# Kernel tuning notes

Hardware: AMD Instinct MI355X
Metric: run time of the kernel (lower is better)

## Reference

```python
import jax, jax.numpy as jnp
import numpy as np
from jax import lax

K = 16        # patch_size / kernel_size
S = 16        # stride
EMB = 768     # embed_dim
CIN = 3


def setup_inputs() -> dict:
    key = jax.random.key(0)
    k1, k2, k3, k4, k5 = jax.random.split(key, 5)
    B, H, W = 64, 384, 384
    pixel_values = jax.random.normal(k1, (B, CIN, H, W), jnp.float32)
    # offset conv: Conv2d(3, 2*K*K, kernel=K, stride=K); small init so offsets stay moderate
    offset_w = jax.random.normal(k2, (2 * K * K, CIN, K, K), jnp.float32) * 0.01
    offset_b = jax.random.normal(k3, (2 * K * K,), jnp.float32) * 0.01
    # deformable projection: DeformConv2d(3, 768, kernel=K, stride=K)
    proj_w = jax.random.normal(k4, (EMB, CIN, K, K), jnp.float32) * 0.02
    proj_b = jax.random.normal(k5, (EMB,), jnp.float32) * 0.02
    return {"pixel_values": pixel_values, "offset_w": offset_w, "offset_b": offset_b,
            "proj_w": proj_w, "proj_b": proj_b}


def _bilinear_gather(img, py, px):
    """img: [B,C,H,W]; py,px: [B,K,K,HO,WO] float sample coords.
    Returns [B,C,K,K,HO,WO] with zero padding outside the image (torchvision semantics)."""
    B, C, H, W = img.shape
    shp = py.shape
    y0 = jnp.floor(py); x0 = jnp.floor(px)
    wy1 = py - y0; wy0 = 1.0 - wy1
    wx1 = px - x0; wx0 = 1.0 - wx1
    imgf = img.reshape(B, C, H * W)

    def corner(yy, xx, w):
        valid = (yy >= 0) & (yy < H) & (xx >= 0) & (xx < W)
        yi = jnp.clip(yy, 0, H - 1).astype(jnp.int32)
        xi = jnp.clip(xx, 0, W - 1).astype(jnp.int32)
        idx = (yi * W + xi).reshape(B, -1)                       # [B, N]
        v = jnp.take_along_axis(imgf, idx[:, None, :], axis=2)   # [B, C, N]
        return v * (jnp.where(valid, w, 0.0)).reshape(B, 1, -1)

    val = (corner(y0, x0, wy0 * wx0) + corner(y0, x0 + 1, wy0 * wx1)
           + corner(y0 + 1, x0, wy1 * wx0) + corner(y0 + 1, x0 + 1, wy1 * wx1))
    return val.reshape((B, C) + shp[1:])


def reference(pixel_values, offset_w, offset_b, proj_w, proj_b):
    B, C, H, W = pixel_values.shape
    HO, WO = H // S, W // S
    # offset conv (dense, stride=patch, VALID padding)
    offset = lax.conv_general_dilated(pixel_values, offset_w, (S, S), 'VALID',
                                      dimension_numbers=('NCHW', 'OIHW', 'NCHW'))
    offset = offset + offset_b[None, :, None, None]              # [B, 2*K*K, HO, WO]
    off = offset.reshape(B, K * K, 2, HO, WO)
    dy = off[:, :, 0].reshape(B, K, K, HO, WO)
    dx = off[:, :, 1].reshape(B, K, K, HO, WO)
    # base sampling grid: p = (ho*S + i + dy, wo*S + j + dx)
    base_y = (jnp.arange(HO, dtype=jnp.float32) * S)[None, None, None, :, None] \
             + jnp.arange(K, dtype=jnp.float32)[None, :, None, None, None]
    base_x = (jnp.arange(WO, dtype=jnp.float32) * S)[None, None, None, None, :] \
             + jnp.arange(K, dtype=jnp.float32)[None, None, :, None, None]
    py = base_y + dy
    px = base_x + dx
    sampled = _bilinear_gather(pixel_values, py, px)             # [B, C, K, K, HO, WO]
    out = jnp.einsum('bcijhw,ocij->bohw', sampled, proj_w) + proj_b[None, :, None, None]
    # flatten(2).transpose(1,2) -> [B, HO*WO, EMB]
    return out.reshape(B, EMB, HO * WO).transpose(0, 2, 1)
```

## Files before the change

### kernel.cpp

```cpp
#include <hip/hip_runtime.h>
#include <stdint.h>

typedef __bf16 bf16x8 __attribute__((ext_vector_type(8)));
typedef float  f32x4  __attribute__((ext_vector_type(4)));

#define HH 384
#define WW 384
#define NPIX (HH*WW)
#define NC 3
#define NPATCH 576
#define EMB 768
#define PLEN 768
#define MLOC 32
#define KSTEPS 24
#define NLOC (64*576)
#define NT1 4
#define NT2 6
#define W1_UNITS (32*KSTEPS*64)
#define W2_UNITS (48*KSTEPS*64)
#define W2_OFF   (W1_UNITS*8)

__device__ __forceinline__ uint16_t f2bf(float f) {
    uint32_t u = __builtin_bit_cast(uint32_t, f);
    u += 0x7FFFu + ((u >> 16) & 1u);
    return (uint16_t)(u >> 16);
}
__device__ __forceinline__ uint32_t pk2(float a, float b) {
    return (uint32_t)f2bf(a) | ((uint32_t)f2bf(b) << 16);
}

__global__ __launch_bounds__(256)
void convert_weights(const float* __restrict__ offw, const float* __restrict__ projw,
                     uint16_t* __restrict__ wz) {
    int u = blockIdx.x * 256 + threadIdx.x;
    const float* src;
    int uu;
    if (u < W1_UNITS) { src = offw; uu = u; }
    else              { src = projw; uu = u - W1_UNITS; }
    int lane = uu & 63;
    int t    = uu >> 6;
    int ks   = t % KSTEPS;
    int nt   = t / KSTEPS;
    int n    = nt * 16 + (lane & 15);
    int k0   = ks * 32 + (lane >> 4) * 8;
    const float4* s4 = (const float4*)(src + (size_t)n * PLEN + k0);
    float4 v0 = s4[0], v1 = s4[1];
    uint4 w;
    w.x = pk2(v0.x, v0.y); w.y = pk2(v0.z, v0.w);
    w.z = pk2(v1.x, v1.y); w.w = pk2(v1.z, v1.w);
    *(uint4*)(wz + (size_t)u * 8) = w;
}

template<bool USE_WS>
__global__ __launch_bounds__(512, 4)
void fused_kernel(const float* __restrict__ pix,
                  const float* __restrict__ offw,
                  const float* __restrict__ offb,
                  const float* __restrict__ projw,
                  const float* __restrict__ projb,
                  const uint16_t* __restrict__ wz,
                  float* __restrict__ out) {
    __shared__ __align__(16) uint16_t As[MLOC][PLEN];

    const int tid  = threadIdx.x;
    const int wv   = tid >> 6;
    const int lane = tid & 63;
    const int lr   = lane & 15;
    const int lg   = lane >> 4;

    int bid = (int)blockIdx.x;
    bid = (bid & 7) * 144 + (bid >> 3);

    const int loc0 = bid * MLOC;
    const int bimg = loc0 / NPATCH;
    const int p0   = loc0 - bimg * NPATCH;
    const float* __restrict__ pb = pix + (size_t)bimg * NC * NPIX;

    #pragma unroll
    for (int uu = 0; uu < 6; ++uu) {
        int unit = tid + uu * 512;
        int loc  = unit / 96;
        int k8   = (unit - loc * 96) * 8;
        int c  = k8 >> 8;
        int i  = (k8 >> 4) & 15;
        int j  = k8 & 15;
        int p  = p0 + loc;
        int ho = p / 24;
        int wo = p - ho * 24;
        const float* g = pb + ((size_t)c * HH + ho * 16 + i) * WW + wo * 16 + j;
        float4 v0 = *(const float4*)g;
        float4 v1 = *(const float4*)(g + 4);
        uint4 w;
        w.x = pk2(v0.x, v0.y); w.y = pk2(v0.z, v0.w);
        w.z = pk2(v1.x, v1.y); w.w = pk2(v1.z, v1.w);
        *(uint4*)&As[loc][k8 ^ ((loc & 7) << 3)] = w;
    }

    const int sw0 = (lr & 7) << 3;

    auto ldb1 = [&](int ntg, int ks) -> bf16x8 {
        if (USE_WS) {
            return *(const bf16x8*)(wz + ((size_t)((ntg * KSTEPS + ks) * 64 + lane)) * 8);
        } else {
            int n = ntg * 16 + lr;
            const float4* s4 = (const float4*)(offw + (size_t)n * PLEN + ks * 32 + lg * 8);
            float4 v0 = s4[0], v1 = s4[1];
            uint4 uq = {pk2(v0.x,v0.y), pk2(v0.z,v0.w), pk2(v1.x,v1.y), pk2(v1.z,v1.w)};
            return __builtin_bit_cast(bf16x8, uq);
        }
    };
    bf16x8 b1a[NT1], b1b[NT1];
    #pragma unroll
    for (int nt = 0; nt < NT1; ++nt) b1a[nt] = ldb1(wv * NT1 + nt, 0);
    __syncthreads();

    f32x4 acc1[2][NT1];
    #pragma unroll
    for (int nt = 0; nt < NT1; ++nt) {
        float bz = offb[(wv * NT1 + nt) * 16 + lr];
        f32x4 z = {bz, bz, bz, bz};
        acc1[0][nt] = z; acc1[1][nt] = z;
    }
    #pragma unroll 1
    for (int ks2 = 0; ks2 < KSTEPS / 2; ++ks2) {
        const int ks0 = ks2 * 2;
        {
            #pragma unroll
            for (int nt = 0; nt < NT1; ++nt) b1b[nt] = ldb1(wv * NT1 + nt, ks0 + 1);
            int ke = (ks0 * 32 + lg * 8) ^ sw0;
            bf16x8 a0 = *(const bf16x8*)&As[lr][ke];
            bf16x8 a1 = *(const bf16x8*)&As[16 + lr][ke];
            __builtin_amdgcn_s_setprio(1);
            #pragma unroll
            for (int nt = 0; nt < NT1; ++nt) {
                acc1[0][nt] = __builtin_amdgcn_mfma_f32_16x16x32_bf16(a0, b1a[nt], acc1[0][nt], 0, 0, 0);
                acc1[1][nt] = __builtin_amdgcn_mfma_f32_16x16x32_bf16(a1, b1a[nt], acc1[1][nt], 0, 0, 0);
            }
            __builtin_amdgcn_s_setprio(0);
        }
        {
            int ksn = (ks0 + 2 < KSTEPS) ? ks0 + 2 : 0;
            #pragma unroll
            for (int nt = 0; nt < NT1; ++nt) b1a[nt] = ldb1(wv * NT1 + nt, ksn);
            int ke = ((ks0 + 1) * 32 + lg * 8) ^ sw0;
            bf16x8 a0 = *(const bf16x8*)&As[lr][ke];
            bf16x8 a1 = *(const bf16x8*)&As[16 + lr][ke];
            __builtin_amdgcn_s_setprio(1);
            #pragma unroll
            for (int nt = 0; nt < NT1; ++nt) {
                acc1[0][nt] = __builtin_amdgcn_mfma_f32_16x16x32_bf16(a0, b1b[nt], acc1[0][nt], 0, 0, 0);
                acc1[1][nt] = __builtin_amdgcn_mfma_f32_16x16x32_bf16(a1, b1b[nt], acc1[1][nt], 0, 0, 0);
            }
            __builtin_amdgcn_s_setprio(0);
        }
    }
    __syncthreads();

    const int even = ((lane & 1) == 0);
    float dyg[2][2][4], dxg[2][2][4];
    #pragma unroll
    for (int nt = 0; nt < NT1; ++nt)
      #pragma unroll
      for (int mt = 0; mt < 2; ++mt)
        #pragma unroll
        for (int r = 0; r < 4; ++r) {
            float v  = acc1[mt][nt][r];
            float pv = __shfl_xor(v, 1);
            if ((nt < 2) == (even != 0)) {
                int s = nt & 1;
                dyg[s][mt][r] = even ? v  : pv;
                dxg[s][mt][r] = even ? pv : v;
            }
        }

    const int ntb  = wv * NT1 + (even ? 0 : 2);
    const int qlow = lr >> 1;
    #pragma unroll
    for (int s = 0; s < 2; ++s) {
        int q  = (ntb + s) * 8 + qlow;
        int qi = q >> 4;
        int qj = q & 15;
        #pragma unroll
        for (int mt = 0; mt < 2; ++mt)
          #pragma unroll
          for (int r = 0; r < 4; ++r) {
            int locl = mt * 16 + lg * 4 + r;
            int p  = p0 + locl;
            int ho = p / 24;
            int wo = p - ho * 24;
            float py = (float)(ho * 16 + qi) + dyg[s][mt][r];
            float px = (float)(wo * 16 + qj) + dxg[s][mt][r];
            float y0f = floorf(py), x0f = floorf(px);
            float wy1 = py - y0f, wy0 = 1.f - wy1;
            float wx1 = px - x0f, wx0 = 1.f - wx1;
            int y0 = (int)y0f, x0 = (int)x0f;
            float s0 = 0.f, s1 = 0.f, s2 = 0.f;
            #pragma unroll
            for (int cy = 0; cy < 2; ++cy) {
                int yy = y0 + cy;
                if ((unsigned)yy < (unsigned)HH) {
                    float wy = cy ? wy1 : wy0;
                    #pragma unroll
                    for (int cx = 0; cx < 2; ++cx) {
                        int xx = x0 + cx;
                        if ((unsigned)xx < (unsigned)WW) {
                            float w = wy * (cx ? wx1 : wx0);
                            const float* cp = pb + yy * WW + xx;
                            s0 += w * cp[0];
                            s1 += w * cp[NPIX];
                            s2 += w * cp[2 * NPIX];
                        }
                    }
                }
            }
            int swl = (locl & 7) << 3;
            As[locl][(      q) ^ swl] = f2bf(s0);
            As[locl][(256 + q) ^ swl] = f2bf(s1);
            As[locl][(512 + q) ^ swl] = f2bf(s2);
          }
    }

    auto ldb2 = [&](int ntg, int ks) -> bf16x8 {
        if (USE_WS) {
            return *(const bf16x8*)(wz + W2_OFF + ((size_t)((ntg * KSTEPS + ks) * 64 + lane)) * 8);
        } else {
            int n = ntg * 16 + lr;
            const float4* s4 = (const float4*)(projw + (size_t)n * PLEN + ks * 32 + lg * 8);
            float4 v0 = s4[0], v1 = s4[1];
            uint4 uq = {pk2(v0.x,v0.y), pk2(v0.z,v0.w), pk2(v1.x,v1.y), pk2(v1.z,v1.w)};
            return __builtin_bit_cast(bf16x8, uq);
        }
    };
    bf16x8 b2a[NT2], b2b[NT2];
    #pragma unroll
    for (int nt = 0; nt < NT2; ++nt) b2a[nt] = ldb2(wv * NT2 + nt, 0);
    __syncthreads();

    f32x4 acc2[2][NT2];
    #pragma unroll
    for (int nt = 0; nt < NT2; ++nt) {
        float bz = projb[(wv * NT2 + nt) * 16 + lr];
        f32x4 z = {bz, bz, bz, bz};
        acc2[0][nt] = z; acc2[1][nt] = z;
    }
    #pragma unroll 1
    for (int ks2 = 0; ks2 < KSTEPS / 2; ++ks2) {
        const int ks0 = ks2 * 2;
        {
            #pragma unroll
            for (int nt = 0; nt < NT2; ++nt) b2b[nt] = ldb2(wv * NT2 + nt, ks0 + 1);
            int ke = (ks0 * 32 + lg * 8) ^ sw0;
            bf16x8 a0 = *(const bf16x8*)&As[lr][ke];
            bf16x8 a1 = *(const bf16x8*)&As[16 + lr][ke];
            __builtin_amdgcn_s_setprio(1);
            #pragma unroll
            for (int nt = 0; nt < NT2; ++nt) {
                acc2[0][nt] = __builtin_amdgcn_mfma_f32_16x16x32_bf16(a0, b2a[nt], acc2[0][nt], 0, 0, 0);
                acc2[1][nt] = __builtin_amdgcn_mfma_f32_16x16x32_bf16(a1, b2a[nt], acc2[1][nt], 0, 0, 0);
            }
            __builtin_amdgcn_s_setprio(0);
        }
        {
            int ksn = (ks0 + 2 < KSTEPS) ? ks0 + 2 : 0;
            #pragma unroll
            for (int nt = 0; nt < NT2; ++nt) b2a[nt] = ldb2(wv * NT2 + nt, ksn);
            int ke = ((ks0 + 1) * 32 + lg * 8) ^ sw0;
            bf16x8 a0 = *(const bf16x8*)&As[lr][ke];
            bf16x8 a1 = *(const bf16x8*)&As[16 + lr][ke];
            __builtin_amdgcn_s_setprio(1);
            #pragma unroll
            for (int nt = 0; nt < NT2; ++nt) {
                acc2[0][nt] = __builtin_amdgcn_mfma_f32_16x16x32_bf16(a0, b2b[nt], acc2[0][nt], 0, 0, 0);
                acc2[1][nt] = __builtin_amdgcn_mfma_f32_16x16x32_bf16(a1, b2b[nt], acc2[1][nt], 0, 0, 0);
            }
            __builtin_amdgcn_s_setprio(0);
        }
    }

    #pragma unroll
    for (int mt = 0; mt < 2; ++mt)
      #pragma unroll
      for (int r = 0; r < 4; ++r) {
        int flat = loc0 + mt * 16 + lg * 4 + r;
        float* op = out + (size_t)flat * EMB;
        #pragma unroll
        for (int nt = 0; nt < NT2; ++nt)
            op[(wv * NT2 + nt) * 16 + lr] = acc2[mt][nt][r];
      }
}

extern "C" void kernel_launch(void* const* d_in, const int* in_sizes, int n_in,
                              void* d_out, int out_size, void* d_ws, size_t ws_size,
                              hipStream_t stream) {
    const float* pix   = (const float*)d_in[0];
    const float* offw  = (const float*)d_in[1];
    const float* offb  = (const float*)d_in[2];
    const float* projw = (const float*)d_in[3];
    const float* projb = (const float*)d_in[4];
    float* out = (float*)d_out;
    uint16_t* wz = (uint16_t*)d_ws;

    const size_t ws_needed = (size_t)(W1_UNITS + W2_UNITS) * 16;
    dim3 grid(NLOC / MLOC);

    if (ws_size >= ws_needed) {
        convert_weights<<<(W1_UNITS + W2_UNITS) / 256, 256, 0, stream>>>(offw, projw, wz);
        fused_kernel<true><<<grid, 512, 0, stream>>>(pix, offw, offb, projw, projb, wz, out);
    } else {
        fused_kernel<false><<<grid, 512, 0, stream>>>(pix, offw, offb, projw, projb, wz, out);
    }
}
```

Baseline: 206.3 us.

## Make fused kernel persistent with atomic tile counter and sample from LDS

Launches a fixed 512-block persistent grid that pulls 32-location tiles from a global atomic counter, reset by a memset each call, instead of one block per tile. Bilinear samples whose corners fall inside the tile's own patches are now read from the bf16 patch copy already staged in LDS rather than from global fp32 pixels. Sampled values are held in registers until after a barrier and then written back to LDS, which removes the earlier barrier placement. This trades tail-effect and launch overhead for an atomic per tile, an extra memset, and lower-precision (bf16) inputs to the sampling.

```diff
diff --git a/kernel.cpp b/kernel.cpp
--- a/kernel.cpp
+++ b/kernel.cpp
@@ -14,11 +14,14 @@
 #define MLOC 32
 #define KSTEPS 24
 #define NLOC (64*576)
+#define NTILES (NLOC/MLOC)
 #define NT1 4
 #define NT2 6
 #define W1_UNITS (32*KSTEPS*64)
 #define W2_UNITS (48*KSTEPS*64)
 #define W2_OFF   (W1_UNITS*8)
+#define CTR_OFF  ((size_t)(W1_UNITS + W2_UNITS) * 16)
+#define PERSIST_BLOCKS 512
 
 __device__ __forceinline__ uint16_t f2bf(float f) {
     uint32_t u = __builtin_bit_cast(uint32_t, f);
@@ -27,6 +30,9 @@
 }
 __device__ __forceinline__ uint32_t pk2(float a, float b) {
     return (uint32_t)f2bf(a) | ((uint32_t)f2bf(b) << 16);
+}
+__device__ __forceinline__ float bf2f(uint16_t u) {
+    return __builtin_bit_cast(float, (uint32_t)u << 16);
 }
 
 __global__ __launch_bounds__(256)
@@ -51,7 +57,7 @@
     *(uint4*)(wz + (size_t)u * 8) = w;
 }
 
-template<bool USE_WS>
+template<bool USE_WS, bool PERSIST>
 __global__ __launch_bounds__(512, 4)
 void fused_kernel(const float* __restrict__ pix,
                   const float* __restrict__ offw,
@@ -59,234 +65,272 @@
                   const float* __restrict__ projw,
                   const float* __restrict__ projb,
                   const uint16_t* __restrict__ wz,
+                  unsigned int* __restrict__ ctr,
                   float* __restrict__ out) {
     __shared__ __align__(16) uint16_t As[MLOC][PLEN];
+    __shared__ int s_tile;
 
     const int tid  = threadIdx.x;
     const int wv   = tid >> 6;
     const int lane = tid & 63;
     const int lr   = lane & 15;
     const int lg   = lane >> 4;
-
-    int bid = (int)blockIdx.x;
-    bid = (bid & 7) * 144 + (bid >> 3);
-
-    const int loc0 = bid * MLOC;
-    const int bimg = loc0 / NPATCH;
-    const int p0   = loc0 - bimg * NPATCH;
-    const float* __restrict__ pb = pix + (size_t)bimg * NC * NPIX;
-
-    #pragma unroll
-    for (int uu = 0; uu < 6; ++uu) {
-        int unit = tid + uu * 512;
-        int loc  = unit / 96;
-        int k8   = (unit - loc * 96) * 8;
-        int c  = k8 >> 8;
-        int i  = (k8 >> 4) & 15;
-        int j  = k8 & 15;
-        int p  = p0 + loc;
-        int ho = p / 24;
-        int wo = p - ho * 24;
-        const float* g = pb + ((size_t)c * HH + ho * 16 + i) * WW + wo * 16 + j;
-        float4 v0 = *(const float4*)g;
-        float4 v1 = *(const float4*)(g + 4);
-        uint4 w;
-        w.x = pk2(v0.x, v0.y); w.y = pk2(v0.z, v0.w);
-        w.z = pk2(v1.x, v1.y); w.w = pk2(v1.z, v1.w);
-        *(uint4*)&As[loc][k8 ^ ((loc & 7) << 3)] = w;
-    }
-
-    const int sw0 = (lr & 7) << 3;
-
-    auto ldb1 = [&](int ntg, int ks) -> bf16x8 {
-        if (USE_WS) {
-            return *(const bf16x8*)(wz + ((size_t)((ntg * KSTEPS + ks) * 64 + lane)) * 8);
+    const int sw0  = (lr & 7) << 3;
+    const int even = ((lane & 1) == 0);
+
+    for (;;) {
+        int tile;
+        if (PERSIST) {
+            if (tid == 0) s_tile = (int)atomicAdd(ctr, 1u);
+            __syncthreads();
+            tile = s_tile;
+            if (tile >= NTILES) break;
         } else {
-            int n = ntg * 16 + lr;
-            const float4* s4 = (const float4*)(offw + (size_t)n * PLEN + ks * 32 + lg * 8);
-            float4 v0 = s4[0], v1 = s4[1];
-            uint4 uq = {pk2(v0.x,v0.y), pk2(v0.z,v0.w), pk2(v1.x,v1.y), pk2(v1.z,v1.w)};
-            return __builtin_bit_cast(bf16x8, uq);
-        }
-    };
-    bf16x8 b1a[NT1], b1b[NT1];
-    #pragma unroll
-    for (int nt = 0; nt < NT1; ++nt) b1a[nt] = ldb1(wv * NT1 + nt, 0);
-    __syncthreads();
-
-    f32x4 acc1[2][NT1];
-    #pragma unroll
-    for (int nt = 0; nt < NT1; ++nt) {
-        float bz = offb[(wv * NT1 + nt) * 16 + lr];
-        f32x4 z = {bz, bz, bz, bz};
-        acc1[0][nt] = z; acc1[1][nt] = z;
-    }
-    #pragma unroll 1
-    for (int ks2 = 0; ks2 < KSTEPS / 2; ++ks2) {
-        const int ks0 = ks2 * 2;
-        {
+            int bid = (int)blockIdx.x;
+            tile = (bid & 7) * 144 + (bid >> 3);
+        }
+
+        const int loc0 = tile * MLOC;
+        const int bimg = loc0 / NPATCH;
+        const int p0   = loc0 - bimg * NPATCH;
+        const float* __restrict__ pb = pix + (size_t)bimg * NC * NPIX;
+
+        #pragma unroll
+        for (int uu = 0; uu < 6; ++uu) {
+            int unit = tid + uu * 512;
+            int loc  = unit / 96;
+            int k8   = (unit - loc * 96) * 8;
+            int c  = k8 >> 8;
+            int i  = (k8 >> 4) & 15;
+            int j  = k8 & 15;
+            int p  = p0 + loc;
+            int ho = p / 24;
+            int wo = p - ho * 24;
+            const float* g = pb + ((size_t)c * HH + ho * 16 + i) * WW + wo * 16 + j;
+            float4 v0 = *(const float4*)g;
+            float4 v1 = *(const float4*)(g + 4);
+            uint4 w;
+            w.x = pk2(v0.x, v0.y); w.y = pk2(v0.z, v0.w);
+            w.z = pk2(v1.x, v1.y); w.w = pk2(v1.z, v1.w);
+            *(uint4*)&As[loc][k8 ^ ((loc & 7) << 3)] = w;
+        }
+
+        auto ldb1 = [&](int ntg, int ks) -> bf16x8 {
+            if (USE_WS) {
+                return *(const bf16x8*)(wz + ((size_t)((ntg * KSTEPS + ks) * 64 + lane)) * 8);
+            } else {
+                int n = ntg * 16 + lr;
+                const float4* s4 = (const float4*)(offw + (size_t)n * PLEN + ks * 32 + lg * 8);
+                float4 v0 = s4[0], v1 = s4[1];
+                uint4 uq = {pk2(v0.x,v0.y), pk2(v0.z,v0.w), pk2(v1.x,v1.y), pk2(v1.z,v1.w)};
+                return __builtin_bit_cast(bf16x8, uq);
+            }
+        };
+        bf16x8 b1a[NT1], b1b[NT1];
+        #pragma unroll
+        for (int nt = 0; nt < NT1; ++nt) b1a[nt] = ldb1(wv * NT1 + nt, 0);
+        __syncthreads();
+
+        f32x4 acc1[2][NT1];
+        #pragma unroll
+        for (int nt = 0; nt < NT1; ++nt) {
+            float bz = offb[(wv * NT1 + nt) * 16 + lr];
+            f32x4 z = {bz, bz, bz, bz};
+            acc1[0][nt] = z; acc1[1][nt] = z;
+        }
+        #pragma unroll 1
+        for (int ks2 = 0; ks2 < KSTEPS / 2; ++ks2) {
+            const int ks0 = ks2 * 2;
+            {
+                #pragma unroll
+                for (int nt = 0; nt < NT1; ++nt) b1b[nt] = ldb1(wv * NT1 + nt, ks0 + 1);
+                int ke = (ks0 * 32 + lg * 8) ^ sw0;
+                bf16x8 a0 = *(const bf16x8*)&As[lr][ke];
+                bf16x8 a1 = *(const bf16x8*)&As[16 + lr][ke];
+                __builtin_amdgcn_s_setprio(1);
+                #pragma unroll
+                for (int nt = 0; nt < NT1; ++nt) {
+                    acc1[0][nt] = __builtin_amdgcn_mfma_f32_16x16x32_bf16(a0, b1a[nt], acc1[0][nt], 0, 0, 0);
+                    acc1[1][nt] = __builtin_amdgcn_mfma_f32_16x16x32_bf16(a1, b1a[nt], acc1[1][nt], 0, 0, 0);
+                }
+                __builtin_amdgcn_s_setprio(0);
+            }
+            {
+                int ksn = (ks0 + 2 < KSTEPS) ? ks0 + 2 : 0;
+                #pragma unroll
+                for (int nt = 0; nt < NT1; ++nt) b1a[nt] = ldb1(wv * NT1 + nt, ksn);
+                int ke = ((ks0 + 1) * 32 + lg * 8) ^ sw0;
+                bf16x8 a0 = *(const bf16x8*)&As[lr][ke];
+                bf16x8 a1 = *(const bf16x8*)&As[16 + lr][ke];
+                __builtin_amdgcn_s_setprio(1);
+                #pragma unroll
+                for (int nt = 0; nt < NT1; ++nt) {
+                    acc1[0][nt] = __builtin_amdgcn_mfma_f32_16x16x32_bf16(a0, b1b[nt], acc1[0][nt], 0, 0, 0);
+                    acc1[1][nt] = __builtin_amdgcn_mfma_f32_16x16x32_bf16(a1, b1b[nt], acc1[1][nt], 0, 0, 0);
+                }
+                __builtin_amdgcn_s_setprio(0);
+            }
+        }
+
+        float dyg[2][2][4], dxg[2][2][4];
+        #pragma unroll
+        for (int nt = 0; nt < NT1; ++nt)
+          #pragma unroll
+          for (int mt = 0; mt < 2; ++mt)
             #pragma unroll
-            for (int nt = 0; nt < NT1; ++nt) b1b[nt] = ldb1(wv * NT1 + nt, ks0 + 1);
-            int ke = (ks0 * 32 + lg * 8) ^ sw0;
-            bf16x8 a0 = *(const bf16x8*)&As[lr][ke];
-            bf16x8 a1 = *(const bf16x8*)&As[16 + lr][ke];
-            __builtin_amdgcn_s_setprio(1);
+            for (int r = 0; r < 4; ++r) {
+                float v  = acc1[mt][nt][r];
+                float pv = __shfl_xor(v, 1);
+                if ((nt < 2) == (even != 0)) {
+                    int s = nt & 1;
+                    dyg[s][mt][r] = even ? v  : pv;
+                    dxg[s][mt][r] = even ? pv : v;
+                }
+            }
+
+        const int ntb  = wv * NT1 + (even ? 0 : 2);
+        const int qlow = lr >> 1;
+        uint32_t smp01[2][2][4];
+        uint32_t smp2 [2][2][4];
+        #pragma unroll
+        for (int s = 0; s < 2; ++s) {
+            int q  = (ntb + s) * 8 + qlow;
+            int qi = q >> 4;
+            int qj = q & 15;
             #pragma unroll
-            for (int nt = 0; nt < NT1; ++nt) {
-                acc1[0][nt] = __builtin_amdgcn_mfma_f32_16x16x32_bf16(a0, b1a[nt], acc1[0][nt], 0, 0, 0);
-                acc1[1][nt] = __builtin_amdgcn_mfma_f32_16x16x32_bf16(a1, b1a[nt], acc1[1][nt], 0, 0, 0);
-            }
-            __builtin_amdgcn_s_setprio(0);
-        }
-        {
-            int ksn = (ks0 + 2 < KSTEPS) ? ks0 + 2 : 0;
+            for (int mt = 0; mt < 2; ++mt)
+              #pragma unroll
+              for (int r = 0; r < 4; ++r) {
+                int locl = mt * 16 + lg * 4 + r;
+                int p  = p0 + locl;
+                int ho = p / 24;
+                int wo = p - ho * 24;
+                float py = (float)(ho * 16 + qi) + dyg[s][mt][r];
+                float px = (float)(wo * 16 + qj) + dxg[s][mt][r];
+                float y0f = floorf(py), x0f = floorf(px);
+                float wy1 = py - y0f, wy0 = 1.f - wy1;
+                float wx1 = px - x0f, wx0 = 1.f - wx1;
+                int y0 = (int)y0f, x0 = (int)x0f;
+                float s0 = 0.f, s1 = 0.f, s2 = 0.f;
+                #pragma unroll
+                for (int cy = 0; cy < 2; ++cy) {
+                    int yy = y0 + cy;
+                    if ((unsigned)yy < (unsigned)HH) {
+                        float wy = cy ? wy1 : wy0;
+                        #pragma unroll
+                        for (int cx = 0; cx < 2; ++cx) {
+                            int xx = x0 + cx;
+                            if ((unsigned)xx < (unsigned)WW) {
+                                float w = wy * (cx ? wx1 : wx0);
+                                int li = ((yy >> 4) * 24 + (xx >> 4)) - p0;
+                                float v0, v1, v2;
+                                if ((unsigned)li < (unsigned)MLOC) {
+                                    int kk  = ((yy & 15) << 4) | (xx & 15);
+                                    int sw2 = (li & 7) << 3;
+                                    v0 = bf2f(As[li][(kk      ) ^ sw2]);
+                                    v1 = bf2f(As[li][(kk + 256) ^ sw2]);
+                                    v2 = bf2f(As[li][(kk + 512) ^ sw2]);
+                                } else {
+                                    const float* cp = pb + yy * WW + xx;
+                                    v0 = cp[0]; v1 = cp[NPIX]; v2 = cp[2 * NPIX];
+                                }
+                                s0 += w * v0; s1 += w * v1; s2 += w * v2;
+                            }
+                        }
+                    }
+                }
+                smp01[s][mt][r] = pk2(s0, s1);
+                smp2 [s][mt][r] = f2bf(s2);
+              }
+        }
+        __syncthreads();
+
+        #pragma unroll
+        for (int s = 0; s < 2; ++s) {
+            int q = (ntb + s) * 8 + qlow;
             #pragma unroll
-            for (int nt = 0; nt < NT1; ++nt) b1a[nt] = ldb1(wv * NT1 + nt, ksn);
-            int ke = ((ks0 + 1) * 32 + lg * 8) ^ sw0;
-            bf16x8 a0 = *(const bf16x8*)&As[lr][ke];
-            bf16x8 a1 = *(const bf16x8*)&As[16 + lr][ke];
-            __builtin_amdgcn_s_setprio(1);
-            #pragma unroll
-            for (int nt = 0; nt < NT1; ++nt) {
-                acc1[0][nt] = __builtin_amdgcn_mfma_f32_16x16x32_bf16(a0, b1b[nt], acc1[0][nt], 0, 0, 0);
-                acc1[1][nt] = __builtin_amdgcn_mfma_f32_16x16x32_bf16(a1, b1b[nt], acc1[1][nt], 0, 0, 0);
-            }
-            __builtin_amdgcn_s_setprio(0);
-        }
-    }
-    __syncthreads();
-
-    const int even = ((lane & 1) == 0);
-    float dyg[2][2][4], dxg[2][2][4];
-    #pragma unroll
-    for (int nt = 0; nt < NT1; ++nt)
-      #pragma unroll
-      for (int mt = 0; mt < 2; ++mt)
-        #pragma unroll
-        for (int r = 0; r < 4; ++r) {
-            float v  = acc1[mt][nt][r];
-            float pv = __shfl_xor(v, 1);
-            if ((nt < 2) == (even != 0)) {
-                int s = nt & 1;
-                dyg[s][mt][r] = even ? v  : pv;
-                dxg[s][mt][r] = even ? pv : v;
-            }
-        }
-
-    const int ntb  = wv * NT1 + (even ? 0 : 2);
-    const int qlow = lr >> 1;
-    #pragma unroll
-    for (int s = 0; s < 2; ++s) {
-        int q  = (ntb + s) * 8 + qlow;
-        int qi = q >> 4;
-        int qj = q & 15;
+            for (int mt = 0; mt < 2; ++mt)
+              #pragma unroll
+              for (int r = 0; r < 4; ++r) {
+                int locl = mt * 16 + lg * 4 + r;
+                int swl = (locl & 7) << 3;
+                uint32_t p01 = smp01[s][mt][r];
+                As[locl][(      q) ^ swl] = (uint16_t)p01;
+                As[locl][(256 + q) ^ swl] = (uint16_t)(p01 >> 16);
+                As[locl][(512 + q) ^ swl] = (uint16_t)smp2[s][mt][r];
+              }
+        }
+
+        auto ldb2 = [&](int ntg, int ks) -> bf16x8 {
+            if (USE_WS) {
+                return *(const bf16x8*)(wz + W2_OFF + ((size_t)((ntg * KSTEPS + ks) * 64 + lane)) * 8);
+            } else {
+                int n = ntg * 16 + lr;
+                const float4* s4 = (const float4*)(projw + (size_t)n * PLEN + ks * 32 + lg * 8);
+                float4 v0 = s4[0], v1 = s4[1];
+                uint4 uq = {pk2(v0.x,v0.y), pk2(v0.z,v0.w), pk2(v1.x,v1.y), pk2(v1.z,v1.w)};
+                return __builtin_bit_cast(bf16x8, uq);
+            }
+        };
+        bf16x8 b2a[NT2], b2b[NT2];
+        #pragma unroll
+        for (int nt = 0; nt < NT2; ++nt) b2a[nt] = ldb2(wv * NT2 + nt, 0);
+        __syncthreads();
+
+        f32x4 acc2[2][NT2];
+        #pragma unroll
+        for (int nt = 0; nt < NT2; ++nt) {
+            float bz = projb[(wv * NT2 + nt) * 16 + lr];
+            f32x4 z = {bz, bz, bz, bz};
+            acc2[0][nt] = z; acc2[1][nt] = z;
+        }
+        #pragma unroll 1
+        for (int ks2 = 0; ks2 < KSTEPS / 2; ++ks2) {
+            const int ks0 = ks2 * 2;
+            {
+                #pragma unroll
+                for (int nt = 0; nt < NT2; ++nt) b2b[nt] = ldb2(wv * NT2 + nt, ks0 + 1);
+                int ke = (ks0 * 32 + lg * 8) ^ sw0;
+                bf16x8 a0 = *(const bf16x8*)&As[lr][ke];
+                bf16x8 a1 = *(const bf16x8*)&As[16 + lr][ke];
+                __builtin_amdgcn_s_setprio(1);
+                #pragma unroll
+                for (int nt = 0; nt < NT2; ++nt) {
+                    acc2[0][nt] = __builtin_amdgcn_mfma_f32_16x16x32_bf16(a0, b2a[nt], acc2[0][nt], 0, 0, 0);
+                    acc2[1][nt] = __builtin_amdgcn_mfma_f32_16x16x32_bf16(a1, b2a[nt], acc2[1][nt], 0, 0, 0);
+                }
+                __builtin_amdgcn_s_setprio(0);
+            }
+            {
+                int ksn = (ks0 + 2 < KSTEPS) ? ks0 + 2 : 0;
+                #pragma unroll
+                for (int nt = 0; nt < NT2; ++nt) b2a[nt] = ldb2(wv * NT2 + nt, ksn);
+                int ke = ((ks0 + 1) * 32 + lg * 8) ^ sw0;
+                bf16x8 a0 = *(const bf16x8*)&As[lr][ke];
+                bf16x8 a1 = *(const bf16x8*)&As[16 + lr][ke];
+                __builtin_amdgcn_s_setprio(1);
+                #pragma unroll
+                for (int nt = 0; nt < NT2; ++nt) {
+                    acc2[0][nt] = __builtin_amdgcn_mfma_f32_16x16x32_bf16(a0, b2b[nt], acc2[0][nt], 0, 0, 0);
+                    acc2[1][nt] = __builtin_amdgcn_mfma_f32_16x16x32_bf16(a1, b2b[nt], acc2[1][nt], 0, 0, 0);
+                }
+                __builtin_amdgcn_s_setprio(0);
+            }
+        }
+
         #pragma unroll
         for (int mt = 0; mt < 2; ++mt)
           #pragma unroll
           for (int r = 0; r < 4; ++r) {
-            int locl = mt * 16 + lg * 4 + r;
-            int p  = p0 + locl;
-            int ho = p / 24;
-            int wo = p - ho * 24;
-            float py = (float)(ho * 16 + qi) + dyg[s][mt][r];
-            float px = (float)(wo * 16 + qj) + dxg[s][mt][r];
-            float y0f = floorf(py), x0f = floorf(px);
-            float wy1 = py - y0f, wy0 = 1.f - wy1;
-            float wx1 = px - x0f, wx0 = 1.f - wx1;
-            int y0 = (int)y0f, x0 = (int)x0f;
-            float s0 = 0.f, s1 = 0.f, s2 = 0.f;
+            int flat = loc0 + mt * 16 + lg * 4 + r;
+            float* op = out + (size_t)flat * EMB;
             #pragma unroll
-            for (int cy = 0; cy < 2; ++cy) {
-                int yy = y0 + cy;
-                if ((unsigned)yy < (unsigned)HH) {
-                    float wy = cy ? wy1 : wy0;
-                    #pragma unroll
-                    for (int cx = 0; cx < 2; ++cx) {
-                        int xx = x0 + cx;
-                        if ((unsigned)xx < (unsigned)WW) {
-                            float w = wy * (cx ? wx1 : wx0);
-                            const float* cp = pb + yy * WW + xx;
-                            s0 += w * cp[0];
-                            s1 += w * cp[NPIX];
-                            s2 += w * cp[2 * NPIX];
-                        }
-                    }
-                }
-            }
-            int swl = (locl & 7) << 3;
-            As[locl][(      q) ^ swl] = f2bf(s0);
-            As[locl][(256 + q) ^ swl] = f2bf(s1);
-            As[locl][(512 + q) ^ swl] = f2bf(s2);
+            for (int nt = 0; nt < NT2; ++nt)
+                op[(wv * NT2 + nt) * 16 + lr] = acc2[mt][nt][r];
           }
+
+        if (!PERSIST) break;
     }
-
-    auto ldb2 = [&](int ntg, int ks) -> bf16x8 {
-        if (USE_WS) {
-            return *(const bf16x8*)(wz + W2_OFF + ((size_t)((ntg * KSTEPS + ks) * 64 + lane)) * 8);
-        } else {
-            int n = ntg * 16 + lr;
-            const float4* s4 = (const float4*)(projw + (size_t)n * PLEN + ks * 32 + lg * 8);
-            float4 v0 = s4[0], v1 = s4[1];
-            uint4 uq = {pk2(v0.x,v0.y), pk2(v0.z,v0.w), pk2(v1.x,v1.y), pk2(v1.z,v1.w)};
-            return __builtin_bit_cast(bf16x8, uq);
-        }
-    };
-    bf16x8 b2a[NT2], b2b[NT2];
-    #pragma unroll
-    for (int nt = 0; nt < NT2; ++nt) b2a[nt] = ldb2(wv * NT2 + nt, 0);
-    __syncthreads();
-
-    f32x4 acc2[2][NT2];
-    #pragma unroll
-    for (int nt = 0; nt < NT2; ++nt) {
-        float bz = projb[(wv * NT2 + nt) * 16 + lr];
-        f32x4 z = {bz, bz, bz, bz};
-        acc2[0][nt] = z; acc2[1][nt] = z;
-    }
-    #pragma unroll 1
-    for (int ks2 = 0; ks2 < KSTEPS / 2; ++ks2) {
-        const int ks0 = ks2 * 2;
-        {
-            #pragma unroll
-            for (int nt = 0; nt < NT2; ++nt) b2b[nt] = ldb2(wv * NT2 + nt, ks0 + 1);
-            int ke = (ks0 * 32 + lg * 8) ^ sw0;
-            bf16x8 a0 = *(const bf16x8*)&As[lr][ke];
-            bf16x8 a1 = *(const bf16x8*)&As[16 + lr][ke];
-            __builtin_amdgcn_s_setprio(1);
-            #pragma unroll
-            for (int nt = 0; nt < NT2; ++nt) {
-                acc2[0][nt] = __builtin_amdgcn_mfma_f32_16x16x32_bf16(a0, b2a[nt], acc2[0][nt], 0, 0, 0);
-                acc2[1][nt] = __builtin_amdgcn_mfma_f32_16x16x32_bf16(a1, b2a[nt], acc2[1][nt], 0, 0, 0);
-            }
-            __builtin_amdgcn_s_setprio(0);
-        }
-        {
-            int ksn = (ks0 + 2 < KSTEPS) ? ks0 + 2 : 0;
-            #pragma unroll
-            for (int nt = 0; nt < NT2; ++nt) b2a[nt] = ldb2(wv * NT2 + nt, ksn);
-            int ke = ((ks0 + 1) * 32 + lg * 8) ^ sw0;
-            bf16x8 a0 = *(const bf16x8*)&As[lr][ke];
-            bf16x8 a1 = *(const bf16x8*)&As[16 + lr][ke];
-            __builtin_amdgcn_s_setprio(1);
-            #pragma unroll
-            for (int nt = 0; nt < NT2; ++nt) {
-                acc2[0][nt] = __builtin_amdgcn_mfma_f32_16x16x32_bf16(a0, b2b[nt], acc2[0][nt], 0, 0, 0);
-                acc2[1][nt] = __builtin_amdgcn_mfma_f32_16x16x32_bf16(a1, b2b[nt], acc2[1][nt], 0, 0, 0);
-            }
-            __builtin_amdgcn_s_setprio(0);
-        }
-    }
-
-    #pragma unroll
-    for (int mt = 0; mt < 2; ++mt)
-      #pragma unroll
-      for (int r = 0; r < 4; ++r) {
-        int flat = loc0 + mt * 16 + lg * 4 + r;
-        float* op = out + (size_t)flat * EMB;
-        #pragma unroll
-        for (int nt = 0; nt < NT2; ++nt)
-            op[(wv * NT2 + nt) * 16 + lr] = acc2[mt][nt][r];
-      }
 }
 
 extern "C" void kernel_launch(void* const* d_in, const int* in_sizes, int n_in,
@@ -300,13 +344,16 @@
     float* out = (float*)d_out;
     uint16_t* wz = (uint16_t*)d_ws;
 
-    const size_t ws_needed = (size_t)(W1_UNITS + W2_UNITS) * 16;
-    dim3 grid(NLOC / MLOC);
+    const size_t ws_needed = CTR_OFF + 64;
 
     if (ws_size >= ws_needed) {
+        unsigned int* ctr = (unsigned int*)((char*)d_ws + CTR_OFF);
+        hipMemsetAsync(ctr, 0, 4, stream);
         convert_weights<<<(W1_UNITS + W2_UNITS) / 256, 256, 0, stream>>>(offw, projw, wz);
-        fused_kernel<true><<<grid, 512, 0, stream>>>(pix, offw, offb, projw, projb, wz, out);
+        fused_kernel<true, true><<<PERSIST_BLOCKS, 512, 0, stream>>>(
+            pix, offw, offb, projw, projb, wz, ctr, out);
     } else {
-        fused_kernel<false><<<grid, 512, 0, stream>>>(pix, offw, offb, projw, projb, wz, out);
+        fused_kernel<false, false><<<NTILES, 512, 0, stream>>>(
+            pix, offw, offb, projw, projb, wz, nullptr, out);
     }
 }
```

Result: slower. 231.8 us (+12.4%).

## Double tile to 64 locations with 1024 threads and add bf16 NHWC pixel copy

Applied to the files above, without the earlier changes.

Raises the per-block tile from 32 to 64 patch locations with 16 waves, so each weight fragment loaded from memory feeds four MFMA row tiles instead of two, which halves weight traffic per output. A separate pre-pass packs the image into a bf16 interleaved-channel layout so that each bilinear corner gather is one 8-byte load instead of three strided fp32 loads. The costs are an extra full-image pass over memory, bf16 rounding of the sampled pixels, a larger LDS tile and fewer blocks for occupancy.

```diff
diff --git a/kernel.cpp b/kernel.cpp
--- a/kernel.cpp
+++ b/kernel.cpp
@@ -11,14 +11,17 @@
 #define NPATCH 576
 #define EMB 768
 #define PLEN 768
-#define MLOC 32
+#define MLOC 64
 #define KSTEPS 24
 #define NLOC (64*576)
-#define NT1 4
-#define NT2 6
+#define NTILES (NLOC/MLOC)
+#define NT1 2
+#define NT2 3
 #define W1_UNITS (32*KSTEPS*64)
 #define W2_UNITS (48*KSTEPS*64)
 #define W2_OFF   (W1_UNITS*8)
+#define PXP_OFF  ((W1_UNITS+W2_UNITS)*8)
+#define NPIX_TOT (64*NPIX)
 
 __device__ __forceinline__ uint16_t f2bf(float f) {
     uint32_t u = __builtin_bit_cast(uint32_t, f);
@@ -27,6 +30,9 @@
 }
 __device__ __forceinline__ uint32_t pk2(float a, float b) {
     return (uint32_t)f2bf(a) | ((uint32_t)f2bf(b) << 16);
+}
+__device__ __forceinline__ float bf2f(uint16_t u) {
+    return __builtin_bit_cast(float, (uint32_t)u << 16);
 }
 
 __global__ __launch_bounds__(256)
@@ -51,8 +57,20 @@
     *(uint4*)(wz + (size_t)u * 8) = w;
 }
 
+__global__ __launch_bounds__(256)
+void nhwc_pass(const float* __restrict__ pix, uint16_t* __restrict__ pxp) {
+    int idx = blockIdx.x * 256 + threadIdx.x;
+    int b  = idx / NPIX;
+    int yx = idx - b * NPIX;
+    const float* p = pix + (size_t)b * NC * NPIX + yx;
+    uint2 w;
+    w.x = pk2(p[0], p[NPIX]);
+    w.y = (uint32_t)f2bf(p[2 * NPIX]);
+    *(uint2*)(pxp + (size_t)idx * 4) = w;
+}
+
 template<bool USE_WS>
-__global__ __launch_bounds__(512, 4)
+__global__ __launch_bounds__(1024, 4)
 void fused_kernel(const float* __restrict__ pix,
                   const float* __restrict__ offw,
                   const float* __restrict__ offb,
@@ -67,18 +85,21 @@
     const int lane = tid & 63;
     const int lr   = lane & 15;
     const int lg   = lane >> 4;
+    const int sw0  = (lr & 7) << 3;
+    const int even = ((lane & 1) == 0);
 
     int bid = (int)blockIdx.x;
-    bid = (bid & 7) * 144 + (bid >> 3);
-
-    const int loc0 = bid * MLOC;
+    const int tile = (bid & 7) * 72 + (bid >> 3);
+
+    const int loc0 = tile * MLOC;
     const int bimg = loc0 / NPATCH;
     const int p0   = loc0 - bimg * NPATCH;
-    const float* __restrict__ pb = pix + (size_t)bimg * NC * NPIX;
+    const float*    __restrict__ pb  = pix + (size_t)bimg * NC * NPIX;
+    const uint16_t* __restrict__ pxp = wz + PXP_OFF + (size_t)bimg * NPIX * 4;
 
     #pragma unroll
     for (int uu = 0; uu < 6; ++uu) {
-        int unit = tid + uu * 512;
+        int unit = tid + uu * 1024;
         int loc  = unit / 96;
         int k8   = (unit - loc * 96) * 8;
         int c  = k8 >> 8;
@@ -96,8 +117,6 @@
         *(uint4*)&As[loc][k8 ^ ((loc & 7) << 3)] = w;
     }
 
-    const int sw0 = (lr & 7) << 3;
-
     auto ldb1 = [&](int ntg, int ks) -> bf16x8 {
         if (USE_WS) {
             return *(const bf16x8*)(wz + ((size_t)((ntg * KSTEPS + ks) * 64 + lane)) * 8);
@@ -114,12 +133,13 @@
     for (int nt = 0; nt < NT1; ++nt) b1a[nt] = ldb1(wv * NT1 + nt, 0);
     __syncthreads();
 
-    f32x4 acc1[2][NT1];
+    f32x4 acc1[4][NT1];
     #pragma unroll
     for (int nt = 0; nt < NT1; ++nt) {
         float bz = offb[(wv * NT1 + nt) * 16 + lr];
         f32x4 z = {bz, bz, bz, bz};
-        acc1[0][nt] = z; acc1[1][nt] = z;
+        #pragma unroll
+        for (int mt = 0; mt < 4; ++mt) acc1[mt][nt] = z;
     }
     #pragma unroll 1
     for (int ks2 = 0; ks2 < KSTEPS / 2; ++ks2) {
@@ -128,13 +148,17 @@
             #pragma unroll
             for (int nt = 0; nt < NT1; ++nt) b1b[nt] = ldb1(wv * NT1 + nt, ks0 + 1);
             int ke = (ks0 * 32 + lg * 8) ^ sw0;
-            bf16x8 a0 = *(const bf16x8*)&As[lr][ke];
+            bf16x8 a0 = *(const bf16x8*)&As[     lr][ke];
             bf16x8 a1 = *(const bf16x8*)&As[16 + lr][ke];
+            bf16x8 a2 = *(const bf16x8*)&As[32 + lr][ke];
+            bf16x8 a3 = *(const bf16x8*)&As[48 + lr][ke];
             __builtin_amdgcn_s_setprio(1);
             #pragma unroll
             for (int nt = 0; nt < NT1; ++nt) {
                 acc1[0][nt] = __builtin_amdgcn_mfma_f32_16x16x32_bf16(a0, b1a[nt], acc1[0][nt], 0, 0, 0);
                 acc1[1][nt] = __builtin_amdgcn_mfma_f32_16x16x32_bf16(a1, b1a[nt], acc1[1][nt], 0, 0, 0);
+                acc1[2][nt] = __builtin_amdgcn_mfma_f32_16x16x32_bf16(a2, b1a[nt], acc1[2][nt], 0, 0, 0);
+                acc1[3][nt] = __builtin_amdgcn_mfma_f32_16x16x32_bf16(a3, b1a[nt], acc1[3][nt], 0, 0, 0);
             }
             __builtin_amdgcn_s_setprio(0);
         }
@@ -143,82 +167,88 @@
             #pragma unroll
             for (int nt = 0; nt < NT1; ++nt) b1a[nt] = ldb1(wv * NT1 + nt, ksn);
             int ke = ((ks0 + 1) * 32 + lg * 8) ^ sw0;
-            bf16x8 a0 = *(const bf16x8*)&As[lr][ke];
+            bf16x8 a0 = *(const bf16x8*)&As[     lr][ke];
             bf16x8 a1 = *(const bf16x8*)&As[16 + lr][ke];
+            bf16x8 a2 = *(const bf16x8*)&As[32 + lr][ke];
+            bf16x8 a3 = *(const bf16x8*)&As[48 + lr][ke];
             __builtin_amdgcn_s_setprio(1);
             #pragma unroll
             for (int nt = 0; nt < NT1; ++nt) {
                 acc1[0][nt] = __builtin_amdgcn_mfma_f32_16x16x32_bf16(a0, b1b[nt], acc1[0][nt], 0, 0, 0);
                 acc1[1][nt] = __builtin_amdgcn_mfma_f32_16x16x32_bf16(a1, b1b[nt], acc1[1][nt], 0, 0, 0);
+                acc1[2][nt] = __builtin_amdgcn_mfma_f32_16x16x32_bf16(a2, b1b[nt], acc1[2][nt], 0, 0, 0);
+                acc1[3][nt] = __builtin_amdgcn_mfma_f32_16x16x32_bf16(a3, b1b[nt], acc1[3][nt], 0, 0, 0);
             }
             __builtin_amdgcn_s_setprio(0);
         }
     }
     __syncthreads();
 
-    const int even = ((lane & 1) == 0);
-    float dyg[2][2][4], dxg[2][2][4];
+    float dyg[4][4], dxg[4][4];
     #pragma unroll
     for (int nt = 0; nt < NT1; ++nt)
       #pragma unroll
-      for (int mt = 0; mt < 2; ++mt)
+      for (int mt = 0; mt < 4; ++mt)
         #pragma unroll
         for (int r = 0; r < 4; ++r) {
             float v  = acc1[mt][nt][r];
             float pv = __shfl_xor(v, 1);
-            if ((nt < 2) == (even != 0)) {
-                int s = nt & 1;
-                dyg[s][mt][r] = even ? v  : pv;
-                dxg[s][mt][r] = even ? pv : v;
-            }
-        }
-
-    const int ntb  = wv * NT1 + (even ? 0 : 2);
+            if ((nt == 0) == (even != 0)) {
+                dyg[mt][r] = even ? v  : pv;
+                dxg[mt][r] = even ? pv : v;
+            }
+        }
+
+    const int ntb  = wv * NT1 + (even ? 0 : 1);
     const int qlow = lr >> 1;
-    #pragma unroll
-    for (int s = 0; s < 2; ++s) {
-        int q  = (ntb + s) * 8 + qlow;
-        int qi = q >> 4;
-        int qj = q & 15;
-        #pragma unroll
-        for (int mt = 0; mt < 2; ++mt)
-          #pragma unroll
-          for (int r = 0; r < 4; ++r) {
-            int locl = mt * 16 + lg * 4 + r;
-            int p  = p0 + locl;
-            int ho = p / 24;
-            int wo = p - ho * 24;
-            float py = (float)(ho * 16 + qi) + dyg[s][mt][r];
-            float px = (float)(wo * 16 + qj) + dxg[s][mt][r];
-            float y0f = floorf(py), x0f = floorf(px);
-            float wy1 = py - y0f, wy0 = 1.f - wy1;
-            float wx1 = px - x0f, wx0 = 1.f - wx1;
-            int y0 = (int)y0f, x0 = (int)x0f;
-            float s0 = 0.f, s1 = 0.f, s2 = 0.f;
-            #pragma unroll
-            for (int cy = 0; cy < 2; ++cy) {
-                int yy = y0 + cy;
-                if ((unsigned)yy < (unsigned)HH) {
-                    float wy = cy ? wy1 : wy0;
-                    #pragma unroll
-                    for (int cx = 0; cx < 2; ++cx) {
-                        int xx = x0 + cx;
-                        if ((unsigned)xx < (unsigned)WW) {
-                            float w = wy * (cx ? wx1 : wx0);
+    const int q    = ntb * 8 + qlow;
+    const int qi   = q >> 4;
+    const int qj   = q & 15;
+    #pragma unroll
+    for (int mt = 0; mt < 4; ++mt)
+      #pragma unroll
+      for (int r = 0; r < 4; ++r) {
+        int locl = mt * 16 + lg * 4 + r;
+        int p  = p0 + locl;
+        int ho = p / 24;
+        int wo = p - ho * 24;
+        float py = (float)(ho * 16 + qi) + dyg[mt][r];
+        float px = (float)(wo * 16 + qj) + dxg[mt][r];
+        float y0f = floorf(py), x0f = floorf(px);
+        float wy1 = py - y0f, wy0 = 1.f - wy1;
+        float wx1 = px - x0f, wx0 = 1.f - wx1;
+        int y0 = (int)y0f, x0 = (int)x0f;
+        float s0 = 0.f, s1 = 0.f, s2 = 0.f;
+        #pragma unroll
+        for (int cy = 0; cy < 2; ++cy) {
+            int yy = y0 + cy;
+            if ((unsigned)yy < (unsigned)HH) {
+                float wy = cy ? wy1 : wy0;
+                #pragma unroll
+                for (int cx = 0; cx < 2; ++cx) {
+                    int xx = x0 + cx;
+                    if ((unsigned)xx < (unsigned)WW) {
+                        float w = wy * (cx ? wx1 : wx0);
+                        float v0, v1, v2;
+                        if (USE_WS) {
+                            uint2 d = *(const uint2*)(pxp + ((size_t)yy * WW + xx) * 4);
+                            v0 = bf2f((uint16_t)d.x);
+                            v1 = bf2f((uint16_t)(d.x >> 16));
+                            v2 = bf2f((uint16_t)d.y);
+                        } else {
                             const float* cp = pb + yy * WW + xx;
-                            s0 += w * cp[0];
-                            s1 += w * cp[NPIX];
-                            s2 += w * cp[2 * NPIX];
+                            v0 = cp[0]; v1 = cp[NPIX]; v2 = cp[2 * NPIX];
                         }
+                        s0 += w * v0; s1 += w * v1; s2 += w * v2;
                     }
                 }
             }
-            int swl = (locl & 7) << 3;
-            As[locl][(      q) ^ swl] = f2bf(s0);
-            As[locl][(256 + q) ^ swl] = f2bf(s1);
-            As[locl][(512 + q) ^ swl] = f2bf(s2);
-          }
-    }
+        }
+        int swl = (locl & 7) << 3;
+        As[locl][(      q) ^ swl] = f2bf(s0);
+        As[locl][(256 + q) ^ swl] = f2bf(s1);
+        As[locl][(512 + q) ^ swl] = f2bf(s2);
+      }
 
     auto ldb2 = [&](int ntg, int ks) -> bf16x8 {
         if (USE_WS) {
@@ -236,12 +266,13 @@
     for (int nt = 0; nt < NT2; ++nt) b2a[nt] = ldb2(wv * NT2 + nt, 0);
     __syncthreads();
 
-    f32x4 acc2[2][NT2];
+    f32x4 acc2[4][NT2];
     #pragma unroll
     for (int nt = 0; nt < NT2; ++nt) {
         float bz = projb[(wv * NT2 + nt) * 16 + lr];
         f32x4 z = {bz, bz, bz, bz};
-        acc2[0][nt] = z; acc2[1][nt] = z;
+        #pragma unroll
+        for (int mt = 0; mt < 4; ++mt) acc2[mt][nt] = z;
     }
     #pragma unroll 1
     for (int ks2 = 0; ks2 < KSTEPS / 2; ++ks2) {
@@ -250,13 +281,17 @@
             #pragma unroll
             for (int nt = 0; nt < NT2; ++nt) b2b[nt] = ldb2(wv * NT2 + nt, ks0 + 1);
             int ke = (ks0 * 32 + lg * 8) ^ sw0;
-            bf16x8 a0 = *(const bf16x8*)&As[lr][ke];
+            bf16x8 a0 = *(const bf16x8*)&As[     lr][ke];
             bf16x8 a1 = *(const bf16x8*)&As[16 + lr][ke];
+            bf16x8 a2 = *(const bf16x8*)&As[32 + lr][ke];
+            bf16x8 a3 = *(const bf16x8*)&As[48 + lr][ke];
             __builtin_amdgcn_s_setprio(1);
             #pragma unroll
             for (int nt = 0; nt < NT2; ++nt) {
                 acc2[0][nt] = __builtin_amdgcn_mfma_f32_16x16x32_bf16(a0, b2a[nt], acc2[0][nt], 0, 0, 0);
                 acc2[1][nt] = __builtin_amdgcn_mfma_f32_16x16x32_bf16(a1, b2a[nt], acc2[1][nt], 0, 0, 0);
+                acc2[2][nt] = __builtin_amdgcn_mfma_f32_16x16x32_bf16(a2, b2a[nt], acc2[2][nt], 0, 0, 0);
+                acc2[3][nt] = __builtin_amdgcn_mfma_f32_16x16x32_bf16(a3, b2a[nt], acc2[3][nt], 0, 0, 0);
             }
             __builtin_amdgcn_s_setprio(0);
         }
@@ -265,20 +300,24 @@
             #pragma unroll
             for (int nt = 0; nt < NT2; ++nt) b2a[nt] = ldb2(wv * NT2 + nt, ksn);
             int ke = ((ks0 + 1) * 32 + lg * 8) ^ sw0;
-            bf16x8 a0 = *(const bf16x8*)&As[lr][ke];
+            bf16x8 a0 = *(const bf16x8*)&As[     lr][ke];
             bf16x8 a1 = *(const bf16x8*)&As[16 + lr][ke];
+            bf16x8 a2 = *(const bf16x8*)&As[32 + lr][ke];
+            bf16x8 a3 = *(const bf16x8*)&As[48 + lr][ke];
             __builtin_amdgcn_s_setprio(1);
             #pragma unroll
             for (int nt = 0; nt < NT2; ++nt) {
                 acc2[0][nt] = __builtin_amdgcn_mfma_f32_16x16x32_bf16(a0, b2b[nt], acc2[0][nt], 0, 0, 0);
                 acc2[1][nt] = __builtin_amdgcn_mfma_f32_16x16x32_bf16(a1, b2b[nt], acc2[1][nt], 0, 0, 0);
+                acc2[2][nt] = __builtin_amdgcn_mfma_f32_16x16x32_bf16(a2, b2b[nt], acc2[2][nt], 0, 0, 0);
+                acc2[3][nt] = __builtin_amdgcn_mfma_f32_16x16x32_bf16(a3, b2b[nt], acc2[3][nt], 0, 0, 0);
             }
             __builtin_amdgcn_s_setprio(0);
         }
     }
 
     #pragma unroll
-    for (int mt = 0; mt < 2; ++mt)
+    for (int mt = 0; mt < 4; ++mt)
       #pragma unroll
       for (int r = 0; r < 4; ++r) {
         int flat = loc0 + mt * 16 + lg * 4 + r;
@@ -300,13 +339,13 @@
     float* out = (float*)d_out;
     uint16_t* wz = (uint16_t*)d_ws;
 
-    const size_t ws_needed = (size_t)(W1_UNITS + W2_UNITS) * 16;
-    dim3 grid(NLOC / MLOC);
+    const size_t ws_needed = (size_t)(W1_UNITS + W2_UNITS) * 16 + (size_t)NPIX_TOT * 8;
 
     if (ws_size >= ws_needed) {
         convert_weights<<<(W1_UNITS + W2_UNITS) / 256, 256, 0, stream>>>(offw, projw, wz);
-        fused_kernel<true><<<grid, 512, 0, stream>>>(pix, offw, offb, projw, projb, wz, out);
+        nhwc_pass<<<NPIX_TOT / 256, 256, 0, stream>>>(pix, wz + PXP_OFF);
+        fused_kernel<true><<<NTILES, 1024, 0, stream>>>(pix, offw, offb, projw, projb, wz, out);
     } else {
-        fused_kernel<false><<<grid, 512, 0, stream>>>(pix, offw, offb, projw, projb, wz, out);
-    }
-}
+        fused_kernel<false><<<NTILES, 1024, 0, stream>>>(pix, offw, offb, projw, projb, wz, out);
+    }
+}
```

Result: slower. 217.0 us (+5.2%).
